# Kernel optimization log

Measured on AMD Instinct MI355X. Metric: run time of the kernel, lower is better.

## Reference

```python
import jax, jax.numpy as jnp
import numpy as np

B, T, L, M = 64, 2000, 400, 80
SIGMA_FACTOR = 0.05
SIGMA_CAP = 10.0
SIGMA_MIN = 1.5
WARMUP_STEPS = 10000
GLOBAL_STEP = 0  # fresh loss module -> progress = 0
ENTROPY_TARGET = 3.5
ATTN_W_START = 1.0
ATTN_W_MIN = 0.2
EPS = 1e-8


def setup_inputs() -> dict:
    key = jax.random.key(0)
    ks = jax.random.split(key, 8)
    mel_out_postnet = jax.random.normal(ks[0], (B, T, M), jnp.float32)
    mel_out = jax.random.normal(ks[1], (B, T, M), jnp.float32)
    gate_out = jax.random.normal(ks[2], (B, T), jnp.float32)
    # alignments: stacked per-step attention, row-normalized like real softmax outputs
    a = jax.random.uniform(ks[3], (B, T, L), jnp.float32)
    alignments = a / jnp.sum(a, axis=-1, keepdims=True)
    mel_target = jax.random.normal(ks[4], (B, T, M), jnp.float32)
    gate_target = jnp.round(jax.random.uniform(ks[5], (B, T), jnp.float32))
    mel_lengths = jax.random.randint(ks[6], (B,), T // 2, T + 1, jnp.int32).at[0].set(T)
    text_lengths = jax.random.randint(ks[7], (B,), L // 2, L + 1, jnp.int32).at[0].set(L)
    return {
        "mel_out_postnet": mel_out_postnet, "mel_out": mel_out, "gate_out": gate_out,
        "alignments": alignments, "mel_target": mel_target, "gate_target": gate_target,
        "mel_lengths": mel_lengths, "text_lengths": text_lengths,
    }


def _diagonal_target(text_lengths):
    # sigma per batch element; global_step=0 -> progress=0 -> sigma = init_sigma
    init_sigma = jnp.clip(text_lengths.astype(jnp.float32) * SIGMA_FACTOR, 3.0, SIGMA_CAP)
    progress = min(1.0, GLOBAL_STEP / float(WARMUP_STEPS))
    sigma = init_sigma - (init_sigma - SIGMA_MIN) * progress  # [B]
    t = jnp.arange(T, dtype=jnp.int32)  # decoder steps
    Lb = text_lengths[:, None]  # [B,1]
    # expected_pos = min(int(t*Lb/T), Lb-1); positive ints -> integer floor div matches trunc
    exp_pos = jnp.minimum((t[None, :] * Lb) // T, Lb - 1).astype(jnp.float32)  # [B,T]
    pos = jnp.arange(L, dtype=jnp.float32)  # [L]
    z = (pos[None, None, :] - exp_pos[:, :, None]) / sigma[:, None, None]
    g = jnp.exp(-0.5 * z * z)  # [B,T,L]
    valid = (pos[None, None, :] < text_lengths[:, None, None].astype(jnp.float32))
    g = g * valid
    return g / (jnp.sum(g, axis=-1, keepdims=True) + EPS)


def reference(mel_out_postnet, mel_out, gate_out, alignments, mel_target,
              gate_target, mel_lengths, text_lengths):
    # masked L1 on mel (mel_target already [B,T,M], matching the torch transpose)
    valid = (jnp.arange(T)[None, :] < mel_lengths[:, None])[:, :, None]  # [B,T,1]
    vf = valid.astype(jnp.float32)
    n_valid = jnp.sum(vf) * M
    mel_loss_1 = jnp.sum(jnp.abs(mel_out - mel_target) * vf) / n_valid
    mel_loss_2 = jnp.sum(jnp.abs(mel_out_postnet - mel_target) * vf) / n_valid
    loss_mel = mel_loss_1 + mel_loss_2

    # BCEWithLogits, mean reduction (stable form)
    x, z_t = gate_out, gate_target
    loss_gate = jnp.mean(jnp.maximum(x, 0.0) - x * z_t + jnp.log1p(jnp.exp(-jnp.abs(x))))

    # guided-attention KL against diagonal Gaussian target
    target = _diagonal_target(text_lengths)  # [B,T,L]
    attn_safe = jnp.maximum(alignments, EPS)
    log_pred = jnp.log(attn_safe)
    kl_pw = jnp.where(target > 0.0, target * (jnp.log(jnp.maximum(target, EPS)) - log_pred), 0.0)
    attention_kl = jnp.sum(kl_pw) / B / T  # batchmean then / T_dec
    attention_kl = jnp.minimum(attention_kl, 150.0)

    # entropy-gated attention weight (python-float in torch -> stop_gradient)
    attn_entropy = jnp.mean(-jnp.sum(attn_safe * log_pred, axis=2))
    ratio = jnp.maximum(attn_entropy / ENTROPY_TARGET, 0.0)
    weight = jnp.where(attn_entropy <= ENTROPY_TARGET,
                       jnp.maximum(ATTN_W_MIN, ATTN_W_START * ratio),
                       ATTN_W_START)
    weight = jax.lax.stop_gradient(weight)

    total_loss = loss_mel + loss_gate + weight * attention_kl
    return (total_loss, loss_mel, loss_gate, attention_kl)
```

## Files before the change

### kernel.cpp

```cpp
#include <hip/hip_runtime.h>
#include <cstddef>
#include <cstdint>

#define B_ 64
#define T_ 2000
#define L_ 400
#define M_ 80
#define EPSF 1e-8f
#define LOG_EPSF -18.420680743952367f

#define NBLK 2048
#define BT_ (B_ * T_)
#define NTHREADS (NBLK * 256)
#define NWAVES (NBLK * 4)
#define L4_ (L_ / 4)
#define TAIL_LANES (L4_ - 64)

__device__ __forceinline__ float waveReduce(float v) {
#pragma unroll
  for (int m = 32; m >= 1; m >>= 1) v += __shfl_xor(v, m, 64);
  return v;
}

__global__ __launch_bounds__(256) void fused_kernel(
    const float4* __restrict__ mo, const float4* __restrict__ mp,
    const float4* __restrict__ mt, const float* __restrict__ gx,
    const float* __restrict__ gz, const float* __restrict__ align,
    const int* __restrict__ mel_lengths, const int* __restrict__ text_lengths,
    double* __restrict__ ws) {
  __shared__ int sh_ml[B_];
  __shared__ int sh_tl[B_];
  if (threadIdx.x < B_) {
    sh_ml[threadIdx.x] = mel_lengths[threadIdx.x];
    sh_tl[threadIdx.x] = text_lengths[threadIdx.x];
  }
  __syncthreads();

  const int tid = blockIdx.x * 256 + threadIdx.x;
  const int lane = threadIdx.x & 63;
  const int wib = threadIdx.x >> 6;
  const int waveId = blockIdx.x * 4 + wib;

  float mel_acc = 0.f, gate_acc = 0.f, kl_acc = 0.f, ent_acc = 0.f;

  auto do_melgate = [&]() {
    const int N4 = B_ * T_ * (M_ / 4);
#pragma unroll 2
    for (int i = tid; i < N4; i += NTHREADS) {
      int row = i / (M_ / 4);
      int b = row / T_;
      int t = row - b * T_;
      if (t < sh_ml[b]) {
        float4 a = mo[i], c = mp[i], d = mt[i];
        mel_acc += fabsf(a.x - d.x) + fabsf(a.y - d.y) + fabsf(a.z - d.z) + fabsf(a.w - d.w)
                 + fabsf(c.x - d.x) + fabsf(c.y - d.y) + fabsf(c.z - d.z) + fabsf(c.w - d.w);
      }
    }
    for (int i = tid; i < BT_; i += NTHREADS) {
      float xv = gx[i], z = gz[i];
      gate_acc += fmaxf(xv, 0.f) - xv * z + log1pf(__expf(-fabsf(xv)));
    }
  };

  auto do_attn = [&]() {
    const float4* a4 = reinterpret_cast<const float4*>(align);
    int p = waveId;
    float4 c0, c1 = make_float4(0.f, 0.f, 0.f, 0.f);
    if (p < BT_) {
      const float4* r = a4 + (size_t)p * L4_;
      c0 = r[lane];
      if (lane < TAIL_LANES) c1 = r[64 + lane];
    }
    while (p < BT_) {
      const int pn = p + NWAVES;
      float4 n0, n1;
      if (pn < BT_) {
        const float4* r = a4 + (size_t)pn * L4_;
        n0 = r[lane];
        if (lane < TAIL_LANES) n1 = r[64 + lane];
      }
      int b = p / T_;
      int t = p - b * T_;
      int Lb = sh_tl[b];
      float sigma = fminf(fmaxf((float)Lb * 0.05f, 3.0f), 10.0f);
      float invsig = 1.0f / sigma;
      int epi = t * Lb / T_;
      int lim = Lb - 1;
      if (epi > lim) epi = lim;
      float ep = (float)epi;

      float S = 0.f, W = 0.f;
      float g0[4], g1[4];
      const int l0 = 4 * lane;
      const float fl0 = (float)l0;
      {
        const float av[4] = {c0.x, c0.y, c0.z, c0.w};
#pragma unroll
        for (int j = 0; j < 4; ++j) {
          float as = fmaxf(av[j], EPSF);
          float lpv = __logf(as);
          ent_acc -= as * lpv;
          float z = (fl0 + (float)j - ep) * invsig;
          float e = -0.5f * z * z;
          float gv = ((l0 + j) < Lb) ? __expf(e) : 0.f;
          g0[j] = gv;
          S += gv;
          W += gv * lpv;
        }
      }
      const int l1 = 256 + 4 * lane;
      const float fl1 = (float)l1;
      if (lane < TAIL_LANES) {
        const float av[4] = {c1.x, c1.y, c1.z, c1.w};
#pragma unroll
        for (int j = 0; j < 4; ++j) {
          float as = fmaxf(av[j], EPSF);
          float lpv = __logf(as);
          ent_acc -= as * lpv;
          float z = (fl1 + (float)j - ep) * invsig;
          float e = -0.5f * z * z;
          float gv = ((l1 + j) < Lb) ? __expf(e) : 0.f;
          g1[j] = gv;
          S += gv;
          W += gv * lpv;
        }
      } else {
#pragma unroll
        for (int j = 0; j < 4; ++j) g1[j] = 0.f;
      }
      float St = waveReduce(S);
      float Se = St + EPSF;
      float inv = 1.0f / Se;
      float logSe = __logf(Se);
      float K = 0.f;
#pragma unroll
      for (int j = 0; j < 4; ++j) {
        float z = (fl0 + (float)j - ep) * invsig;
        float e = -0.5f * z * z;
        float lt = fmaxf(e - logSe, LOG_EPSF);
        K += g0[j] * lt;
      }
#pragma unroll
      for (int j = 0; j < 4; ++j) {
        float z = (fl1 + (float)j - ep) * invsig;
        float e = -0.5f * z * z;
        float lt = fmaxf(e - logSe, LOG_EPSF);
        K += g1[j] * lt;
      }
      kl_acc += inv * (K - W);
      p = pn; c0 = n0; c1 = n1;
    }
  };

  if (blockIdx.x & 1) { do_attn(); do_melgate(); }
  else                { do_melgate(); do_attn(); }

  float w0 = waveReduce(mel_acc);
  float w1 = waveReduce(gate_acc);
  float w2 = waveReduce(kl_acc);
  float w3 = waveReduce(ent_acc);
  __shared__ double sh[4][4];
  if (lane == 0) {
    sh[wib][0] = (double)w0; sh[wib][1] = (double)w1;
    sh[wib][2] = (double)w2; sh[wib][3] = (double)w3;
  }
  __syncthreads();
  if (threadIdx.x == 0) {
    ws[blockIdx.x]            = sh[0][0] + sh[1][0] + sh[2][0] + sh[3][0];
    ws[NBLK + blockIdx.x]     = sh[0][1] + sh[1][1] + sh[2][1] + sh[3][1];
    ws[2 * NBLK + blockIdx.x] = sh[0][2] + sh[1][2] + sh[2][2] + sh[3][2];
    ws[3 * NBLK + blockIdx.x] = sh[0][3] + sh[1][3] + sh[2][3] + sh[3][3];
  }
}

__device__ double segSum(const double* __restrict__ p, int n, double* sh) {
  double a = 0.0;
  for (int i = threadIdx.x; i < n; i += 256) a += p[i];
  sh[threadIdx.x] = a;
  __syncthreads();
  for (int s = 128; s > 0; s >>= 1) {
    if ((int)threadIdx.x < s) sh[threadIdx.x] += sh[threadIdx.x + s];
    __syncthreads();
  }
  double r = sh[0];
  __syncthreads();
  return r;
}

__global__ __launch_bounds__(256) void finalize_kernel(
    const double* __restrict__ ws, const int* __restrict__ mel_lengths,
    float* __restrict__ out) {
  __shared__ double sh[256];
  double mel_sum  = segSum(ws, NBLK, sh);
  double gate_sum = segSum(ws + NBLK, NBLK, sh);
  double kl_sum   = segSum(ws + 2 * NBLK, NBLK, sh);
  double ent_sum  = segSum(ws + 3 * NBLK, NBLK, sh);
  if (threadIdx.x == 0) {
    long nv = 0;
    for (int b = 0; b < B_; ++b) nv += mel_lengths[b];
    double n_valid = (double)nv * (double)M_;
    float loss_mel  = (float)(mel_sum / n_valid);
    float loss_gate = (float)(gate_sum / (double)(B_ * T_));
    float kl  = (float)(kl_sum / (double)(B_ * T_));
    kl = fminf(kl, 150.0f);
    float ent = (float)(ent_sum / (double)(B_ * T_));
    float ratio = fmaxf(ent / 3.5f, 0.0f);
    float weight = (ent <= 3.5f) ? fmaxf(0.2f, 1.0f * ratio) : 1.0f;
    out[0] = loss_mel + loss_gate + weight * kl;
    out[1] = loss_mel;
    out[2] = loss_gate;
    out[3] = kl;
  }
}

extern "C" void kernel_launch(void* const* d_in, const int* in_sizes, int n_in,
                              void* d_out, int out_size, void* d_ws, size_t ws_size,
                              hipStream_t stream) {
  const float* mel_out_postnet = (const float*)d_in[0];
  const float* mel_out         = (const float*)d_in[1];
  const float* gate_out        = (const float*)d_in[2];
  const float* alignments      = (const float*)d_in[3];
  const float* mel_target      = (const float*)d_in[4];
  const float* gate_target     = (const float*)d_in[5];
  const int*   mel_lengths     = (const int*)d_in[6];
  const int*   text_lengths    = (const int*)d_in[7];
  float* out = (float*)d_out;
  double* ws = (double*)d_ws;

  fused_kernel<<<dim3(NBLK), dim3(256), 0, stream>>>(
      (const float4*)mel_out, (const float4*)mel_out_postnet,
      (const float4*)mel_target, gate_out, gate_target,
      alignments, mel_lengths, text_lengths, ws);
  finalize_kernel<<<dim3(1), dim3(256), 0, stream>>>(ws, mel_lengths, out);
}
```

Measured before the change: 392.2 us.

## Interleave mel loads with attention rows in one fixed-trip loop, use base-2 math

The separate mel/gate and attention phases are merged into one loop with a fixed trip count. Each iteration issues nontemporal mel loads next to the prefetched alignment row, so both streams are in flight together. The Gaussian and log terms now use the native exp2/log2 intrinsics, with a single ln2 rescale in finalize. The tail-chunk Gaussian is skipped when it lies more than about 13.6 sigma from the diagonal, and the gate loss is computed once per thread. The risks are the extra live registers and the skip condition, which relies on the Gaussian underflowing to zero in that region.

```diff
diff --git a/kernel.cpp b/kernel.cpp
--- a/kernel.cpp
+++ b/kernel.cpp
@@ -7,14 +7,24 @@
 #define L_ 400
 #define M_ 80
 #define EPSF 1e-8f
-#define LOG_EPSF -18.420680743952367f
+#define LOG2_EPSF -26.575424759098897f
+#define LN2 0.6931471805599453
 
 #define NBLK 2048
 #define BT_ (B_ * T_)
 #define NTHREADS (NBLK * 256)
 #define NWAVES (NBLK * 4)
-#define L4_ (L_ / 4)
-#define TAIL_LANES (L4_ - 64)
+#define L4_ 100
+#define TAIL_LANES 36
+#define N4_ (B_ * T_ * (M_ / 4))
+#define NCH_ (N4_ / 64)
+#define MAXK 16
+#define MELK 5
+
+typedef float vf4 __attribute__((ext_vector_type(4)));
+
+#define LOG2F(x) __builtin_amdgcn_logf(x)
+#define EXP2F(x) __builtin_amdgcn_exp2f(x)
 
 __device__ __forceinline__ float waveReduce(float v) {
 #pragma unroll
@@ -23,8 +33,8 @@
 }
 
 __global__ __launch_bounds__(256) void fused_kernel(
-    const float4* __restrict__ mo, const float4* __restrict__ mp,
-    const float4* __restrict__ mt, const float* __restrict__ gx,
+    const vf4* __restrict__ mo, const vf4* __restrict__ mp,
+    const vf4* __restrict__ mt, const float* __restrict__ gx,
     const float* __restrict__ gz, const float* __restrict__ align,
     const int* __restrict__ mel_lengths, const int* __restrict__ text_lengths,
     double* __restrict__ ws) {
@@ -41,44 +51,51 @@
   const int wib = threadIdx.x >> 6;
   const int waveId = blockIdx.x * 4 + wib;
 
-  float mel_acc = 0.f, gate_acc = 0.f, kl_acc = 0.f, ent_acc = 0.f;
-
-  auto do_melgate = [&]() {
-    const int N4 = B_ * T_ * (M_ / 4);
-#pragma unroll 2
-    for (int i = tid; i < N4; i += NTHREADS) {
-      int row = i / (M_ / 4);
-      int b = row / T_;
-      int t = row - b * T_;
-      if (t < sh_ml[b]) {
-        float4 a = mo[i], c = mp[i], d = mt[i];
-        mel_acc += fabsf(a.x - d.x) + fabsf(a.y - d.y) + fabsf(a.z - d.z) + fabsf(a.w - d.w)
-                 + fabsf(c.x - d.x) + fabsf(c.y - d.y) + fabsf(c.z - d.z) + fabsf(c.w - d.w);
-      }
-    }
-    for (int i = tid; i < BT_; i += NTHREADS) {
-      float xv = gx[i], z = gz[i];
-      gate_acc += fmaxf(xv, 0.f) - xv * z + log1pf(__expf(-fabsf(xv)));
-    }
-  };
-
-  auto do_attn = [&]() {
-    const float4* a4 = reinterpret_cast<const float4*>(align);
-    int p = waveId;
-    float4 c0, c1 = make_float4(0.f, 0.f, 0.f, 0.f);
-    if (p < BT_) {
-      const float4* r = a4 + (size_t)p * L4_;
-      c0 = r[lane];
-      if (lane < TAIL_LANES) c1 = r[64 + lane];
-    }
-    while (p < BT_) {
-      const int pn = p + NWAVES;
-      float4 n0, n1;
-      if (pn < BT_) {
-        const float4* r = a4 + (size_t)pn * L4_;
-        n0 = r[lane];
-        if (lane < TAIL_LANES) n1 = r[64 + lane];
-      }
+  float mel_acc = 0.f, gate_acc = 0.f, kl_acc = 0.f, ent2_acc = 0.f;
+
+  if (tid < BT_) {
+    float xv = gx[tid], z = gz[tid];
+    gate_acc = fmaxf(xv, 0.f) - xv * z + log1pf(__expf(-fabsf(xv)));
+  }
+
+  const float4* a4 = reinterpret_cast<const float4*>(align);
+  const float fl0 = (float)(4 * lane);
+
+  float4 c0, c1 = make_float4(0.f, 0.f, 0.f, 0.f);
+  {
+    const float4* r = a4 + (size_t)waveId * L4_;
+    c0 = r[lane];
+    if (lane < TAIL_LANES) c1 = r[64 + lane];
+  }
+
+#pragma unroll 1
+  for (int k = 0; k < MAXK; ++k) {
+    const int p = waveId + k * NWAVES;
+    const bool pv = (p < BT_);
+
+    float4 n0 = make_float4(0.f, 0.f, 0.f, 0.f), n1 = n0;
+    const int pn = p + NWAVES;
+    if (pn < BT_) {
+      const float4* r = a4 + (size_t)pn * L4_;
+      n0 = r[lane];
+      if (lane < TAIL_LANES) n1 = r[64 + lane];
+    }
+
+    vf4 ma, mb, md;
+    int mi = 0;
+    bool mv = false;
+    if (k < MELK) {
+      int ch = waveId + k * NWAVES;
+      mv = (ch < NCH_);
+      if (mv) {
+        mi = ch * 64 + lane;
+        ma = __builtin_nontemporal_load(&mo[mi]);
+        mb = __builtin_nontemporal_load(&mp[mi]);
+        md = __builtin_nontemporal_load(&mt[mi]);
+      }
+    }
+
+    if (pv) {
       int b = p / T_;
       int t = p - b * T_;
       int Lb = sh_tl[b];
@@ -88,77 +105,92 @@
       int lim = Lb - 1;
       if (epi > lim) epi = lim;
       float ep = (float)epi;
-
-      float S = 0.f, W = 0.f;
-      float g0[4], g1[4];
-      const int l0 = 4 * lane;
-      const float fl0 = (float)l0;
+      float cg = -0.7213475204444817f * invsig * invsig;
+      float d0 = fl0 - ep;
+      float d1 = d0 + 256.f;
+
+      float S = 0.f, W2 = 0.f;
+      float gs[8];
+#pragma unroll
+      for (int j = 4; j < 8; ++j) gs[j] = 0.f;
+
       {
         const float av[4] = {c0.x, c0.y, c0.z, c0.w};
 #pragma unroll
         for (int j = 0; j < 4; ++j) {
           float as = fmaxf(av[j], EPSF);
-          float lpv = __logf(as);
-          ent_acc -= as * lpv;
-          float z = (fl0 + (float)j - ep) * invsig;
-          float e = -0.5f * z * z;
-          float gv = ((l0 + j) < Lb) ? __expf(e) : 0.f;
-          g0[j] = gv;
+          float lp2 = LOG2F(as);
+          ent2_acc = fmaf(-as, lp2, ent2_acc);
+          float dj = d0 + (float)j;
+          float e2 = dj * dj * cg;
+          float gv = EXP2F(e2);
+          gv = ((4 * lane + j) < Lb) ? gv : 0.f;
+          gs[j] = gv;
           S += gv;
-          W += gv * lpv;
+          W2 = fmaf(gv, lp2, W2);
         }
       }
-      const int l1 = 256 + 4 * lane;
-      const float fl1 = (float)l1;
+      const bool c1w = (256.f - ep) < 13.6f * sigma;
       if (lane < TAIL_LANES) {
         const float av[4] = {c1.x, c1.y, c1.z, c1.w};
 #pragma unroll
         for (int j = 0; j < 4; ++j) {
           float as = fmaxf(av[j], EPSF);
-          float lpv = __logf(as);
-          ent_acc -= as * lpv;
-          float z = (fl1 + (float)j - ep) * invsig;
-          float e = -0.5f * z * z;
-          float gv = ((l1 + j) < Lb) ? __expf(e) : 0.f;
-          g1[j] = gv;
-          S += gv;
-          W += gv * lpv;
+          float lp2 = LOG2F(as);
+          ent2_acc = fmaf(-as, lp2, ent2_acc);
+          if (c1w) {
+            float dj = d1 + (float)j;
+            float e2 = dj * dj * cg;
+            float gv = EXP2F(e2);
+            gv = ((256 + 4 * lane + j) < Lb) ? gv : 0.f;
+            gs[4 + j] = gv;
+            S += gv;
+            W2 = fmaf(gv, lp2, W2);
+          }
         }
-      } else {
-#pragma unroll
-        for (int j = 0; j < 4; ++j) g1[j] = 0.f;
-      }
+      }
+
       float St = waveReduce(S);
       float Se = St + EPSF;
       float inv = 1.0f / Se;
-      float logSe = __logf(Se);
-      float K = 0.f;
+      float lSe2 = LOG2F(Se);
+
+      float K2 = 0.f;
 #pragma unroll
       for (int j = 0; j < 4; ++j) {
-        float z = (fl0 + (float)j - ep) * invsig;
-        float e = -0.5f * z * z;
-        float lt = fmaxf(e - logSe, LOG_EPSF);
-        K += g0[j] * lt;
-      }
-#pragma unroll
-      for (int j = 0; j < 4; ++j) {
-        float z = (fl1 + (float)j - ep) * invsig;
-        float e = -0.5f * z * z;
-        float lt = fmaxf(e - logSe, LOG_EPSF);
-        K += g1[j] * lt;
-      }
-      kl_acc += inv * (K - W);
-      p = pn; c0 = n0; c1 = n1;
-    }
-  };
-
-  if (blockIdx.x & 1) { do_attn(); do_melgate(); }
-  else                { do_melgate(); do_attn(); }
+        float dj = d0 + (float)j;
+        float e2 = dj * dj * cg;
+        K2 = fmaf(gs[j], fmaxf(e2 - lSe2, LOG2_EPSF), K2);
+      }
+      if (c1w) {
+#pragma unroll
+        for (int j = 0; j < 4; ++j) {
+          float dj = d1 + (float)j;
+          float e2 = dj * dj * cg;
+          K2 = fmaf(gs[4 + j], fmaxf(e2 - lSe2, LOG2_EPSF), K2);
+        }
+      }
+      kl_acc = fmaf(inv, K2 - W2, kl_acc);
+    }
+
+    if (mv) {
+      int row = mi / 20;
+      int b2 = row / T_;
+      int t2 = row - b2 * T_;
+      float s8 = fabsf(ma.x - md.x) + fabsf(ma.y - md.y) + fabsf(ma.z - md.z) +
+                 fabsf(ma.w - md.w) + fabsf(mb.x - md.x) + fabsf(mb.y - md.y) +
+                 fabsf(mb.z - md.z) + fabsf(mb.w - md.w);
+      mel_acc += (t2 < sh_ml[b2]) ? s8 : 0.f;
+    }
+
+    c0 = n0;
+    c1 = n1;
+  }
 
   float w0 = waveReduce(mel_acc);
   float w1 = waveReduce(gate_acc);
   float w2 = waveReduce(kl_acc);
-  float w3 = waveReduce(ent_acc);
+  float w3 = waveReduce(ent2_acc);
   __shared__ double sh[4][4];
   if (lane == 0) {
     sh[wib][0] = (double)w0; sh[wib][1] = (double)w1;
@@ -201,9 +233,9 @@
     double n_valid = (double)nv * (double)M_;
     float loss_mel  = (float)(mel_sum / n_valid);
     float loss_gate = (float)(gate_sum / (double)(B_ * T_));
-    float kl  = (float)(kl_sum / (double)(B_ * T_));
+    float kl  = (float)(kl_sum * LN2 / (double)(B_ * T_));
     kl = fminf(kl, 150.0f);
-    float ent = (float)(ent_sum / (double)(B_ * T_));
+    float ent = (float)(ent_sum * LN2 / (double)(B_ * T_));
     float ratio = fmaxf(ent / 3.5f, 0.0f);
     float weight = (ent <= 3.5f) ? fmaxf(0.2f, 1.0f * ratio) : 1.0f;
     out[0] = loss_mel + loss_gate + weight * kl;
@@ -228,8 +260,8 @@
   double* ws = (double*)d_ws;
 
   fused_kernel<<<dim3(NBLK), dim3(256), 0, stream>>>(
-      (const float4*)mel_out, (const float4*)mel_out_postnet,
-      (const float4*)mel_target, gate_out, gate_target,
+      (const vf4*)mel_out, (const vf4*)mel_out_postnet,
+      (const vf4*)mel_target, gate_out, gate_target,
       alignments, mel_lengths, text_lengths, ws);
   finalize_kernel<<<dim3(1), dim3(256), 0, stream>>>(ws, mel_lengths, out);
 }
```

New measurement: 386.1 us. About the same (-1.6%).
